# Optimization experiments

Measured on AMD Instinct MI355X. Metric: run time of the kernel, lower is better.

## Reference

```python
import jax, jax.numpy as jnp
import numpy as np
from jax import lax

D_MODEL = 1024
D_INNER = 2048   # expand * d_model
D_STATE = 16
D_CONV = 4
DT_RANK = 64     # ceil(d_model / 16)
B_SZ, L_SEQ = 2, 2048


def setup_inputs() -> dict:
    key = jax.random.key(0)
    ks = jax.random.split(key, 12)
    s = lambda *sh: 1.0 / np.sqrt(sh[-1])
    inp = {
        "x": jax.random.normal(ks[0], (B_SZ, L_SEQ, D_MODEL), jnp.float32),
        "in_proj_w": jax.random.normal(ks[1], (2 * D_INNER, D_MODEL), jnp.float32) * s(D_MODEL),
        "conv_w": jax.random.normal(ks[2], (D_INNER, 1, D_CONV), jnp.float32) * 0.3,
        "conv_b": jax.random.normal(ks[3], (D_INNER,), jnp.float32) * 0.05,
        "x_proj_w": jax.random.normal(ks[4], (DT_RANK + 2 * D_STATE, D_INNER), jnp.float32) * s(D_INNER),
        "dt_proj_w": jax.random.normal(ks[5], (D_INNER, DT_RANK), jnp.float32) * s(DT_RANK),
        "dt_proj_b": jnp.log(jnp.exp(jax.random.uniform(ks[6], (D_INNER,), jnp.float32, 1e-3, 1e-1)) - 1.0),
        "A_log": jnp.log(jnp.broadcast_to(jnp.arange(1, D_STATE + 1, dtype=jnp.float32), (D_INNER, D_STATE))),
        "D": jnp.ones((D_INNER,), jnp.float32),
        "out_proj_w": jax.random.normal(ks[7], (D_MODEL, D_INNER), jnp.float32) * s(D_INNER),
        "ln_w": jnp.ones((D_MODEL,), jnp.float32),
        "ln_b": jnp.zeros((D_MODEL,), jnp.float32),
    }
    return inp


def _mamba(x, in_proj_w, conv_w, conv_b, x_proj_w, dt_proj_w, dt_proj_b, A_log, D, out_proj_w):
    # x: [B, L, d_model]
    xz = x @ in_proj_w.T                             # [B, L, 2*d_inner]
    u, z = jnp.split(xz, 2, axis=-1)                 # [B, L, d_inner] each
    # depthwise causal conv1d along L
    u_c = jnp.swapaxes(u, 1, 2)                      # [B, d_inner, L]
    u_c = lax.conv_general_dilated(
        u_c, conv_w, window_strides=(1,), padding=[(D_CONV - 1, 0)],
        feature_group_count=D_INNER, dimension_numbers=("NCH", "OIH", "NCH"))
    u_c = u_c + conv_b[None, :, None]
    u_c = jax.nn.silu(jnp.swapaxes(u_c, 1, 2))       # [B, L, d_inner]
    # input-dependent dt, B, C
    x_dbl = u_c @ x_proj_w.T                         # [B, L, dt_rank + 2*d_state]
    dt_lr = x_dbl[..., :DT_RANK]
    Bm = x_dbl[..., DT_RANK:DT_RANK + D_STATE]       # [B, L, d_state]
    Cm = x_dbl[..., DT_RANK + D_STATE:]              # [B, L, d_state]
    dt = jax.nn.softplus(dt_lr @ dt_proj_w.T + dt_proj_b)  # [B, L, d_inner]
    A = -jnp.exp(A_log)                              # [d_inner, d_state]

    def step(h, inputs):
        dt_t, b_t, c_t, u_t = inputs                 # [B,d_inner],[B,N],[B,N],[B,d_inner]
        dA = jnp.exp(dt_t[:, :, None] * A)           # [B, d_inner, N]
        h = h * dA + (dt_t * u_t)[:, :, None] * b_t[:, None, :]
        y_t = jnp.einsum("bdn,bn->bd", h, c_t)
        return h, y_t

    h0 = jnp.zeros((x.shape[0], D_INNER, D_STATE), x.dtype)
    xs = (jnp.swapaxes(dt, 0, 1), jnp.swapaxes(Bm, 0, 1),
          jnp.swapaxes(Cm, 0, 1), jnp.swapaxes(u_c, 0, 1))
    _, ys = lax.scan(step, h0, xs)                   # ys: [L, B, d_inner]
    y = jnp.swapaxes(ys, 0, 1) + u_c * D             # skip connection D*u
    y = y * jax.nn.silu(z)                           # gate
    return y @ out_proj_w.T                          # [B, L, d_model]


def _layernorm(x, w, b, eps=1e-5):
    mu = jnp.mean(x, axis=-1, keepdims=True)
    var = jnp.mean(jnp.square(x - mu), axis=-1, keepdims=True)
    return (x - mu) * lax.rsqrt(var + eps) * w + b


def reference(x, in_proj_w, conv_w, conv_b, x_proj_w, dt_proj_w, dt_proj_b,
              A_log, D, out_proj_w, ln_w, ln_b):
    y = _mamba(x, in_proj_w, conv_w, conv_b, x_proj_w, dt_proj_w, dt_proj_b,
               A_log, D, out_proj_w)
    return _layernorm(y + x, ln_w, ln_b)  # dropout_level=0 -> identity
```

## Files before the change

### kernel.cpp

```cpp
#include <hip/hip_runtime.h>
#include <hip/hip_bf16.h>
#include <math.h>

#define DEV static __device__ __forceinline__

typedef __hip_bfloat16 bf16;
typedef __attribute__((ext_vector_type(8))) short bf16x8;
typedef __attribute__((ext_vector_type(4))) short bf16x4;
typedef __attribute__((ext_vector_type(4))) float f32x4;

static constexpr int D_MODEL = 1024;
static constexpr int D_INNER = 2048;
static constexpr int D_STATE = 16;
static constexpr int DT_RANK = 64;
static constexpr int B_SZ   = 2;
static constexpr int L_SEQ  = 2048;
static constexpr int T_TOK  = B_SZ * L_SEQ;
static constexpr int LC     = 64;
static constexpr int NC     = L_SEQ / LC;
static constexpr int NXP    = DT_RANK + 2 * D_STATE;
static constexpr int KSPLIT = 8;

static constexpr int P_CONVW = 0;
static constexpr int P_CONVB = 8192;
static constexpr int P_DTB   = 10240;
static constexpr int P_ALOG  = 12288;
static constexpr int P_DW    = 45056;
static constexpr int P_LNW   = 47104;
static constexpr int P_LNB   = 48128;
static constexpr int P_TOT   = 49152;

DEV float bf2f(bf16 x) { return __bfloat162float(x); }
DEV bf16  f2bf(float x) { return __float2bfloat16(x); }
DEV float sigmoidf_(float x) { return 1.0f / (1.0f + __expf(-x)); }
DEV float s2f(short s) { bf16 b; __builtin_memcpy(&b, &s, 2); return bf2f(b); }
DEV short f2s(float x) { bf16 b = f2bf(x); short s; __builtin_memcpy(&s, &b, 2); return s; }

DEV bool probe_f32(const unsigned short* probe) { return probe[1] == 0; }

DEV void async_copy16(const void* g, void* l) {
  __builtin_amdgcn_global_load_lds(
      (const __attribute__((address_space(1))) void*)g,
      (__attribute__((address_space(3))) void*)l, 16, 0, 0);
}

template <int N>
DEV void vm_wait() {
  if constexpr (N == 6) asm volatile("s_waitcnt vmcnt(6)" ::: "memory");
  else                  asm volatile("s_waitcnt vmcnt(0)" ::: "memory");
}

__global__ void cvt_all(const void* s0, const void* s1, const void* s2,
                        const void* s3, const void* s4,
                        const void* s5, const void* s6, const void* s7,
                        const void* s8, const void* s9, const void* s10,
                        const void* s11,
                        bf16* d0, bf16* d1, bf16* d2, bf16* d3, bf16* d4,
                        float* params,
                        const unsigned short* __restrict__ probe)
{
  long i = (long)(blockIdx.x * 256 + threadIdx.x) * 4;
  const void* src; long off;
  bf16* dstb = nullptr; float* dstf = nullptr;
  if      (i <  4194304) { src = s0;  dstb = d0; off = i; }
  else if (i <  8388608) { src = s1;  dstb = d1; off = i - 4194304; }
  else if (i <  8585216) { src = s2;  dstb = d2; off = i - 8388608; }
  else if (i <  8716288) { src = s3;  dstb = d3; off = i - 8585216; }
  else if (i < 10813440) { src = s4;  dstb = d4; off = i - 8716288; }
  else if (i < 10821632) { src = s5;  dstf = params + P_CONVW; off = i - 10813440; }
  else if (i < 10823680) { src = s6;  dstf = params + P_CONVB; off = i - 10821632; }
  else if (i < 10825728) { src = s7;  dstf = params + P_DTB;   off = i - 10823680; }
  else if (i < 10858496) { src = s8;  dstf = params + P_ALOG;  off = i - 10825728; }
  else if (i < 10860544) { src = s9;  dstf = params + P_DW;    off = i - 10858496; }
  else if (i < 10861568) { src = s10; dstf = params + P_LNW;   off = i - 10860544; }
  else if (i < 10862592) { src = s11; dstf = params + P_LNB;   off = i - 10861568; }
  else return;
  bool isf32 = probe_f32(probe);
  float v[4];
  if (isf32) {
    float4 t = *(const float4*)((const float*)src + off);
    v[0] = t.x; v[1] = t.y; v[2] = t.z; v[3] = t.w;
  } else {
    short4 t = *(const short4*)((const bf16*)src + off);
    v[0] = s2f(t.x); v[1] = s2f(t.y); v[2] = s2f(t.z); v[3] = s2f(t.w);
  }
  if (dstb) {
    #pragma unroll
    for (int k = 0; k < 4; ++k) dstb[off + k] = f2bf(v[k]);
  } else {
    #pragma unroll
    for (int k = 0; k < 4; ++k) dstf[off + k] = v[k];
  }
}

static constexpr int SLOT = 48 * 1024;
static constexpr int BOFF = 32 * 1024;

DEV void stage_A(const bf16* __restrict__ A, int ld, int bm, int k0,
                 char* slot, int tid) {
  #pragma unroll
  for (int j = 0; j < 4; ++j) {
    int p   = j * 8192 + tid * 16;
    int row = p >> 7;
    int ck  = ((p >> 4) & 7) ^ (row & 7);
    async_copy16(A + (size_t)(bm + row) * ld + k0 + ck * 8,
                 slot + j * 8192 + (tid >> 6) * 1024);
  }
}

DEV void stage_B(const bf16* __restrict__ B, int ld, int bn, int k0,
                 char* slot, int tid) {
  #pragma unroll
  for (int j = 0; j < 2; ++j) {
    int p   = j * 8192 + tid * 16;
    int row = p >> 7;
    int ck  = ((p >> 4) & 7) ^ (row & 7);
    async_copy16(B + (size_t)(bn + row) * ld + k0 + ck * 8,
                 slot + BOFF + j * 8192 + (tid >> 6) * 1024);
  }
}

template <int MODE>
DEV void gemm_pipe(const bf16* __restrict__ A, const bf16* __restrict__ B,
                   int M, int K, int ld,
                   void* __restrict__ o0, void* __restrict__ o1)
{
  __shared__ __align__(16) char ring[3 * SLOT];
  if (MODE == 3) {
    A += (size_t)blockIdx.z * K;
    B += (size_t)blockIdx.z * K;
  }
  const int tid  = threadIdx.x;
  const int wave = tid >> 6;
  const int lane = tid & 63;
  const int bm = blockIdx.x * 256;
  const int bn = blockIdx.y * 128;
  const int wm = (wave >> 1) * 64;
  const int wn = (wave & 1) * 64;
  const int fr = lane & 15;
  const int fq = lane >> 4;
  const int NT = K / 64;

  f32x4 acc[4][4];
  #pragma unroll
  for (int i = 0; i < 4; ++i)
    #pragma unroll
    for (int j = 0; j < 4; ++j)
      #pragma unroll
      for (int r = 0; r < 4; ++r) acc[i][j][r] = 0.0f;

  stage_A(A, ld, bm, 0,  ring,        tid);
  stage_B(B, ld, bn, 0,  ring,        tid);
  stage_A(A, ld, bm, 64, ring + SLOT, tid);
  stage_B(B, ld, bn, 64, ring + SLOT, tid);

  int scur = 0;
  #pragma unroll 1
  for (int tk = 0; tk < NT; ++tk) {
    if (tk < NT - 1) vm_wait<6>();
    else             vm_wait<0>();
    __builtin_amdgcn_sched_barrier(0);
    __builtin_amdgcn_s_barrier();
    __builtin_amdgcn_sched_barrier(0);

    const char* sa = ring + scur * SLOT;
    int snxt = scur + 2; if (snxt >= 3) snxt -= 3;
    char* sn = ring + snxt * SLOT;

    bf16x8 af[4][2], bg[2][2];
    #pragma unroll
    for (int mi = 0; mi < 4; ++mi)
      #pragma unroll
      for (int kk = 0; kk < 2; ++kk) {
        int row = wm + mi * 16 + fr;
        af[mi][kk] = *(const bf16x8*)(sa + row * 128 + (((kk * 4 + fq) ^ (fr & 7)) * 16));
      }
    #pragma unroll
    for (int ni = 0; ni < 2; ++ni)
      #pragma unroll
      for (int kk = 0; kk < 2; ++kk) {
        int row = wn + ni * 16 + fr;
        bg[ni][kk] = *(const bf16x8*)(sa + BOFF + row * 128 + (((kk * 4 + fq) ^ (fr & 7)) * 16));
      }
    __builtin_amdgcn_sched_barrier(0);
    if (tk + 2 < NT) stage_A(A, ld, bm, (tk + 2) * 64, sn, tid);
    __builtin_amdgcn_sched_barrier(0);
    asm volatile("s_waitcnt lgkmcnt(0)" ::: "memory");
    __builtin_amdgcn_sched_barrier(0);
    __builtin_amdgcn_s_setprio(1);
    #pragma unroll
    for (int kk = 0; kk < 2; ++kk)
      #pragma unroll
      for (int mi = 0; mi < 4; ++mi)
        #pragma unroll
        for (int ni = 0; ni < 2; ++ni)
          acc[mi][ni] = __builtin_amdgcn_mfma_f32_16x16x32_bf16(af[mi][kk], bg[ni][kk], acc[mi][ni], 0, 0, 0);
    __builtin_amdgcn_s_setprio(0);
    __builtin_amdgcn_sched_barrier(0);

    bf16x8 bh[2][2];
    #pragma unroll
    for (int ni = 0; ni < 2; ++ni)
      #pragma unroll
      for (int kk = 0; kk < 2; ++kk) {
        int row = wn + (ni + 2) * 16 + fr;
        bh[ni][kk] = *(const bf16x8*)(sa + BOFF + row * 128 + (((kk * 4 + fq) ^ (fr & 7)) * 16));
      }
    __builtin_amdgcn_sched_barrier(0);
    if (tk + 2 < NT) stage_B(B, ld, bn, (tk + 2) * 64, sn, tid);
    __builtin_amdgcn_sched_barrier(0);
    asm volatile("s_waitcnt lgkmcnt(0)" ::: "memory");
    __builtin_amdgcn_sched_barrier(0);
    __builtin_amdgcn_s_setprio(1);
    #pragma unroll
    for (int kk = 0; kk < 2; ++kk)
      #pragma unroll
      for (int mi = 0; mi < 4; ++mi)
        #pragma unroll
        for (int ni = 0; ni < 2; ++ni)
          acc[mi][ni + 2] = __builtin_amdgcn_mfma_f32_16x16x32_bf16(af[mi][kk], bh[ni][kk], acc[mi][ni + 2], 0, 0, 0);
    __builtin_amdgcn_s_setprio(0);
    __builtin_amdgcn_sched_barrier(0);

    scur = (scur + 1 == 3) ? 0 : scur + 1;
  }

  const int er = (lane >> 4) * 4;
  const int ec = lane & 15;
  #pragma unroll
  for (int mi = 0; mi < 4; ++mi) {
    #pragma unroll
    for (int ni = 0; ni < 4; ++ni) {
      #pragma unroll
      for (int r = 0; r < 4; ++r) {
        int row = bm + wm + mi * 16 + er + r;
        int col = bn + wn + ni * 16 + ec;
        float v = acc[mi][ni][r];
        if (MODE == 0) {
          if (col < D_INNER) ((bf16*)o0)[(size_t)row * D_INNER + col] = f2bf(v);
          else               ((bf16*)o1)[(size_t)row * D_INNER + (col - D_INNER)] = f2bf(v * sigmoidf_(v));
        } else {
          ((bf16*)o0)[((size_t)blockIdx.z * M + row) * D_MODEL + col] = f2bf(v);
        }
      }
    }
  }
}

template <int MODE>
DEV void gemm_body32(const bf16* __restrict__ A, const bf16* __restrict__ B,
                     int M, int N, int K, int ld,
                     void* __restrict__ o0, const void* __restrict__ e0)
{
  __shared__ __align__(16) bf16 As[128 * 32];
  __shared__ __align__(16) bf16 Bs[128 * 32];
  if (MODE == 1) {
    A += (size_t)blockIdx.z * K;
    B += (size_t)blockIdx.z * K;
  }
  const int tid  = threadIdx.x;
  const int wave = tid >> 6;
  const int lane = tid & 63;
  const int bm = blockIdx.x * 128;
  const int bn = blockIdx.y * 128;
  const int wm = (wave >> 1) * 64;
  const int wn = (wave & 1) * 64;

  f32x4 acc[4][4];
  #pragma unroll
  for (int i = 0; i < 4; ++i)
    #pragma unroll
    for (int j = 0; j < 4; ++j)
      #pragma unroll
      for (int r = 0; r < 4; ++r) acc[i][j][r] = 0.0f;

  const int ar0 = tid >> 2;
  const int ar1 = ar0 + 64;
  const int ac  = (tid & 3) * 8;
  const int fr = lane & 15;
  const int fk = (lane >> 4) * 8;

  for (int k0 = 0; k0 < K; k0 += 32) {
    bf16x8 a0 = *(const bf16x8*)(A + (size_t)(bm + ar0) * ld + k0 + ac);
    bf16x8 a1 = *(const bf16x8*)(A + (size_t)(bm + ar1) * ld + k0 + ac);
    int r0 = bn + ar0; if (r0 > N - 1) r0 = N - 1;
    int r1 = bn + ar1; if (r1 > N - 1) r1 = N - 1;
    bf16x8 b0 = *(const bf16x8*)(B + (size_t)r0 * ld + k0 + ac);
    bf16x8 b1 = *(const bf16x8*)(B + (size_t)r1 * ld + k0 + ac);
    __syncthreads();
    *(bf16x8*)(As + ar0 * 32 + ac) = a0;
    *(bf16x8*)(As + ar1 * 32 + ac) = a1;
    *(bf16x8*)(Bs + ar0 * 32 + ac) = b0;
    *(bf16x8*)(Bs + ar1 * 32 + ac) = b1;
    __syncthreads();

    bf16x8 af[4], bg[4];
    #pragma unroll
    for (int mi = 0; mi < 4; ++mi)
      af[mi] = *(const bf16x8*)(As + (wm + mi * 16 + fr) * 32 + fk);
    #pragma unroll
    for (int ni = 0; ni < 4; ++ni)
      bg[ni] = *(const bf16x8*)(Bs + (wn + ni * 16 + fr) * 32 + fk);
    #pragma unroll
    for (int mi = 0; mi < 4; ++mi)
      #pragma unroll
      for (int ni = 0; ni < 4; ++ni)
        acc[mi][ni] = __builtin_amdgcn_mfma_f32_16x16x32_bf16(af[mi], bg[ni], acc[mi][ni], 0, 0, 0);
  }

  const int er = (lane >> 4) * 4;
  const int ec = lane & 15;
  #pragma unroll
  for (int mi = 0; mi < 4; ++mi) {
    #pragma unroll
    for (int ni = 0; ni < 4; ++ni) {
      #pragma unroll
      for (int r = 0; r < 4; ++r) {
        int row = bm + wm + mi * 16 + er + r;
        int col = bn + wn + ni * 16 + ec;
        if (col >= N) continue;
        float v = acc[mi][ni][r];
        if (MODE == 1) {
          ((float*)o0)[((size_t)blockIdx.z * M + row) * N + col] = v;
        } else {
          v += ((const float*)e0)[col];
          float sp = (v > 15.0f) ? v : __logf(1.0f + __expf(v));
          ((bf16*)o0)[(size_t)row * D_INNER + col] = f2bf(sp);
        }
      }
    }
  }
}

__global__ void __launch_bounds__(512) k_inproj(const bf16* A, const bf16* B,
    void* o0, void* o1) {
  gemm_pipe<0>(A, B, T_TOK, D_MODEL, D_MODEL, o0, o1);
}
__global__ void __launch_bounds__(512) k_outproj(const bf16* A, const bf16* B,
    void* o0) {
  gemm_pipe<3>(A, B, T_TOK, D_INNER / 2, D_INNER, o0, nullptr);
}
__global__ void __launch_bounds__(256) k_xproj(const bf16* A, const bf16* B,
    void* o0) {
  gemm_body32<1>(A, B, T_TOK, NXP, D_INNER / KSPLIT, D_INNER, o0, nullptr);
}
__global__ void __launch_bounds__(256) k_dtproj(const bf16* A, const bf16* B,
    void* o0, const void* e0) {
  gemm_body32<2>(A, B, T_TOK, D_INNER, DT_RANK, DT_RANK, o0, e0);
}

__global__ void xproj_post(const float* __restrict__ partials,
                           bf16* __restrict__ dtlr,
                           float* __restrict__ Bbuf,
                           float* __restrict__ Cbuf)
{
  int i = blockIdx.x * 256 + threadIdx.x;
  int col = i % NXP;
  int row = i / NXP;
  float s = 0.0f;
  #pragma unroll
  for (int kz = 0; kz < KSPLIT; ++kz)
    s += partials[((size_t)kz * T_TOK + row) * NXP + col];
  if      (col < DT_RANK)            dtlr[(size_t)row * DT_RANK + col] = f2bf(s);
  else if (col < DT_RANK + D_STATE)  Bbuf[(size_t)row * D_STATE + (col - DT_RANK)] = s;
  else                               Cbuf[(size_t)row * D_STATE + (col - DT_RANK - D_STATE)] = s;
}

__global__ void conv_silu_kernel(const bf16* __restrict__ u_pre,
                                 const float* __restrict__ cw,
                                 const float* __restrict__ cb,
                                 bf16* __restrict__ uc_bf)
{
  int idx = blockIdx.x * 256 + threadIdx.x;
  int d4 = (idx * 4) & (D_INNER - 1);
  int t  = (idx * 4) >> 11;
  int l  = t & (L_SEQ - 1);
  float4 bias = *(const float4*)(cb + d4);
  float acc[4] = {bias.x, bias.y, bias.z, bias.w};
  float4 wv[4];
  #pragma unroll
  for (int i = 0; i < 4; ++i) wv[i] = *(const float4*)(cw + (d4 + i) * 4);
  #pragma unroll
  for (int w = 0; w < 4; ++w) {
    if (l - 3 + w >= 0) {
      bf16x4 u = *(const bf16x4*)(u_pre + (size_t)(t - 3 + w) * D_INNER + d4);
      float uf[4];
      #pragma unroll
      for (int i = 0; i < 4; ++i) { short su = u[i]; uf[i] = s2f(su); }
      acc[0] += uf[0] * ((const float*)&wv[0])[w];
      acc[1] += uf[1] * ((const float*)&wv[1])[w];
      acc[2] += uf[2] * ((const float*)&wv[2])[w];
      acc[3] += uf[3] * ((const float*)&wv[3])[w];
    }
  }
  bf16x4 out;
  #pragma unroll
  for (int i = 0; i < 4; ++i) out[i] = f2s(acc[i] * sigmoidf_(acc[i]));
  *(bf16x4*)(uc_bf + (size_t)t * D_INNER + d4) = out;
}

DEV void load_Ad(const float* A_log, int d, float* Ad, bool& fast) {
  fast = true;
  #pragma unroll
  for (int n = 0; n < 16; ++n) {
    Ad[n] = -__expf(A_log[d * 16 + n]);
    fast = fast && (fabsf(Ad[n] + (float)(n + 1)) < 1e-3f * (n + 1));
  }
}
DEV void compute_decay(bool fast, float dtv, const float* Ad, float* dec) {
  if (fast) {
    float e1 = __expf(-dtv);
    float en = e1;
    #pragma unroll
    for (int n = 0; n < 16; ++n) { dec[n] = en; en *= e1; }
  } else {
    #pragma unroll
    for (int n = 0; n < 16; ++n) dec[n] = __expf(Ad[n] * dtv);
  }
}

__global__ __launch_bounds__(256) void scan_pass1(
    const bf16* __restrict__ dt, const bf16* __restrict__ uc_bf,
    const float* __restrict__ Bbuf, const float* __restrict__ A_log,
    float* __restrict__ hend, float* __restrict__ sumdt)
{
  __shared__ float Bs4[LC * D_STATE];
  __shared__ bf16 dts[16 * 256];
  __shared__ bf16 uts[16 * 256];
  int bid = blockIdx.x;
  int tid = threadIdx.x;
  int dt8 = bid & 7;
  int c = (bid >> 3) & (NC - 1);
  int b = bid >> 8;
  int d0 = dt8 * 256;
  int d  = d0 + tid;
  int t0g = b * L_SEQ + c * LC;

  ((f32x4*)Bs4)[tid] = ((const f32x4*)(Bbuf + (size_t)t0g * D_STATE))[tid];

  float Ad[16], h[16];
  bool fast;
  load_Ad(A_log, d, Ad, fast);
  #pragma unroll
  for (int n = 0; n < 16; ++n) h[n] = 0.0f;
  float sdt = 0.0f;

  for (int sub = 0; sub < 4; ++sub) {
    __syncthreads();
    #pragma unroll
    for (int rep = 0; rep < 2; ++rep) {
      int idx = rep * 256 + tid;
      int row = idx >> 5;
      int col = (idx & 31) * 8;
      size_t src = (size_t)(t0g + sub * 16 + row) * D_INNER + d0 + col;
      *(bf16x8*)(dts + row * 256 + col) = *(const bf16x8*)(dt + src);
      *(bf16x8*)(uts + row * 256 + col) = *(const bf16x8*)(uc_bf + src);
    }
    __syncthreads();
    for (int t = 0; t < 16; ++t) {
      float dtv = bf2f(dts[t * 256 + tid]);
      float uv  = bf2f(uts[t * 256 + tid]);
      float su  = dtv * uv;
      sdt += dtv;
      float dec[16];
      compute_decay(fast, dtv, Ad, dec);
      const float* Bp = Bs4 + (sub * 16 + t) * 16;
      #pragma unroll
      for (int n = 0; n < 16; ++n)
        h[n] = h[n] * dec[n] + su * Bp[n];
    }
  }
  size_t base = ((size_t)(b * NC + c) * D_INNER + d) * 16;
  #pragma unroll
  for (int q = 0; q < 4; ++q)
    *(f32x4*)(hend + base + q * 4) = *(f32x4*)(h + q * 4);
  sumdt[(size_t)(b * NC + c) * D_INNER + d] = sdt;
}

__global__ __launch_bounds__(256) void scan_pass2(
    float* __restrict__ hend, const float* __restrict__ sumdt,
    const float* __restrict__ A_log)
{
  __shared__ float Ms[4][64];
  __shared__ float Es[4][64];
  int bid = blockIdx.x;
  int tid = threadIdx.x;
  int cg   = tid >> 6;
  int lane = tid & 63;
  int dloc = lane >> 4;
  int n    = lane & 15;
  int b     = bid >> 9;
  int d     = (bid & 511) * 4 + dloc;

  float a = -__expf(A_log[d * 16 + n]);

  float Ml[8], El[8];
  float M = 1.0f, E = 0.0f;
  #pragma unroll
  for (int j = 0; j < 8; ++j) {
    int c = cg * 8 + j;
    size_t sbase = (size_t)(b * NC + c) * D_INNER + d;
    float m = __expf(a * sumdt[sbase]);
    float e = hend[sbase * 16 + n];
    Ml[j] = M; El[j] = E;
    M = m * M;
    E = m * E + e;
  }
  Ms[cg][lane] = M;
  Es[cg][lane] = E;
  __syncthreads();
  float Ep = 0.0f;
  for (int g = 0; g < cg; ++g) {
    float Mg = Ms[g][lane], Eg = Es[g][lane];
    Ep = Mg * Ep + Eg;
  }
  #pragma unroll
  for (int j = 0; j < 8; ++j) {
    int c = cg * 8 + j;
    size_t sbase = (size_t)(b * NC + c) * D_INNER + d;
    hend[sbase * 16 + n] = Ml[j] * Ep + El[j];
  }
}

__global__ __launch_bounds__(256) void scan_pass3(
    const bf16* __restrict__ dt, const bf16* __restrict__ uc_bf,
    const float* __restrict__ Bbuf, const float* __restrict__ Cbuf,
    const bf16* __restrict__ z_silu, const float* __restrict__ hstart,
    const float* __restrict__ A_log, const float* __restrict__ Dw,
    bf16* __restrict__ y_bf)
{
  __shared__ float Bs4[LC * D_STATE];
  __shared__ float Cs4[LC * D_STATE];
  __shared__ bf16 dts[16 * 256];
  __shared__ bf16 uts[16 * 256];
  __shared__ bf16 zts[16 * 256];
  int bid = blockIdx.x;
  int tid = threadIdx.x;
  int dt8 = bid & 7;
  int c = (bid >> 3) & (NC - 1);
  int b = bid >> 8;
  int d0 = dt8 * 256;
  int d  = d0 + tid;
  int t0g = b * L_SEQ + c * LC;

  ((f32x4*)Bs4)[tid] = ((const f32x4*)(Bbuf + (size_t)t0g * D_STATE))[tid];
  ((f32x4*)Cs4)[tid] = ((const f32x4*)(Cbuf + (size_t)t0g * D_STATE))[tid];

  float Ad[16], h[16];
  bool fast;
  load_Ad(A_log, d, Ad, fast);
  size_t base = ((size_t)(b * NC + c) * D_INNER + d) * 16;
  #pragma unroll
  for (int q = 0; q < 4; ++q)
    *(f32x4*)(h + q * 4) = *(const f32x4*)(hstart + base + q * 4);
  float Dv = Dw[d];

  for (int sub = 0; sub < 4; ++sub) {
    __syncthreads();
    #pragma unroll
    for (int rep = 0; rep < 2; ++rep) {
      int idx = rep * 256 + tid;
      int row = idx >> 5;
      int col = (idx & 31) * 8;
      size_t src = (size_t)(t0g + sub * 16 + row) * D_INNER + d0 + col;
      *(bf16x8*)(dts + row * 256 + col) = *(const bf16x8*)(dt + src);
      *(bf16x8*)(uts + row * 256 + col) = *(const bf16x8*)(uc_bf + src);
      *(bf16x8*)(zts + row * 256 + col) = *(const bf16x8*)(z_silu + src);
    }
    __syncthreads();
    for (int t = 0; t < 16; ++t) {
      float dtv = bf2f(dts[t * 256 + tid]);
      float uv  = bf2f(uts[t * 256 + tid]);
      float zv  = bf2f(zts[t * 256 + tid]);
      float su  = dtv * uv;
      float dec[16];
      compute_decay(fast, dtv, Ad, dec);
      const float* Bp = Bs4 + (sub * 16 + t) * 16;
      const float* Cp = Cs4 + (sub * 16 + t) * 16;
      float y = 0.0f;
      #pragma unroll
      for (int n = 0; n < 16; ++n) {
        h[n] = h[n] * dec[n] + su * Bp[n];
        y += h[n] * Cp[n];
      }
      y = (y + uv * Dv) * zv;
      y_bf[(size_t)(t0g + sub * 16 + t) * D_INNER + d] = f2bf(y);
    }
  }
}

__global__ void ln_kernel(const bf16* __restrict__ parts,
                          const bf16* __restrict__ x_bf,
                          const float* __restrict__ w,
                          const float* __restrict__ bia,
                          void* __restrict__ out,
                          const unsigned short* __restrict__ probe)
{
  int t = blockIdx.x;
  int tid = threadIdx.x;
  const bf16* p0 = parts + (size_t)t * D_MODEL;
  const bf16* p1 = parts + ((size_t)T_TOK + t) * D_MODEL;
  const bf16* xr = x_bf + (size_t)t * D_MODEL;
  float v[4];
  float s = 0.0f, q = 0.0f;
  #pragma unroll
  for (int k = 0; k < 4; ++k) {
    int col = tid + k * 256;
    v[k] = bf2f(p0[col]) + bf2f(p1[col]) + bf2f(xr[col]);
    s += v[k]; q += v[k] * v[k];
  }
  #pragma unroll
  for (int off = 32; off >= 1; off >>= 1) {
    s += __shfl_down(s, off);
    q += __shfl_down(q, off);
  }
  __shared__ float red[8];
  __shared__ float mv[2];
  int wave = tid >> 6, lane = tid & 63;
  if (lane == 0) { red[wave] = s; red[4 + wave] = q; }
  __syncthreads();
  if (tid == 0) {
    float S = red[0] + red[1] + red[2] + red[3];
    float Q = red[4] + red[5] + red[6] + red[7];
    float mu = S * (1.0f / D_MODEL);
    float var = Q * (1.0f / D_MODEL) - mu * mu;
    mv[0] = mu; mv[1] = rsqrtf(var + 1e-5f);
  }
  __syncthreads();
  float mu = mv[0], rs = mv[1];
  bool isf32 = probe_f32(probe);
  #pragma unroll
  for (int k = 0; k < 4; ++k) {
    int col = tid + k * 256;
    float r = (v[k] - mu) * rs * w[col] + bia[col];
    if (isf32) ((float*)out)[(size_t)t * D_MODEL + col] = r;
    else       ((bf16*) out)[(size_t)t * D_MODEL + col] = f2bf(r);
  }
}

extern "C" void kernel_launch(void* const* d_in, const int* in_sizes, int n_in,
                              void* d_out, int out_size, void* d_ws, size_t ws_size,
                              hipStream_t stream)
{
  const void* x        = d_in[0];
  const void* in_w     = d_in[1];
  const void* conv_w   = d_in[2];
  const void* conv_b   = d_in[3];
  const void* xproj_w  = d_in[4];
  const void* dtproj_w = d_in[5];
  const void* dtproj_b = d_in[6];
  const void* A_log    = d_in[7];
  const void* Dw       = d_in[8];
  const void* out_w    = d_in[9];
  const void* ln_w     = d_in[10];
  const void* ln_b     = d_in[11];
  const unsigned short* probe = (const unsigned short*)A_log;

  char* p = (char*)d_ws;
  auto alloc = [&](size_t bytes) { char* r = p; p += (bytes + 255) & ~255ull; return r; };
  bf16*  x_bf   = (bf16*) alloc((size_t)T_TOK * D_MODEL * 2);
  bf16*  inw_bf = (bf16*) alloc((size_t)2 * D_INNER * D_MODEL * 2);
  bf16*  xpw_bf = (bf16*) alloc((size_t)NXP * D_INNER * 2);
  bf16*  dtw_bf = (bf16*) alloc((size_t)D_INNER * DT_RANK * 2);
  bf16*  outw_bf= (bf16*) alloc((size_t)D_MODEL * D_INNER * 2);
  float* params = (float*)alloc((size_t)P_TOT * 4);
  bf16*  u_pre  = (bf16*) alloc((size_t)T_TOK * D_INNER * 2);
  bf16*  z_silu = (bf16*) alloc((size_t)T_TOK * D_INNER * 2);
  bf16*  uc_bf  = (bf16*) alloc((size_t)T_TOK * D_INNER * 2);
  bf16*  dtlr   = (bf16*) alloc((size_t)T_TOK * DT_RANK * 2);
  float* Bbuf   = (float*)alloc((size_t)T_TOK * D_STATE * 4);
  float* Cbuf   = (float*)alloc((size_t)T_TOK * D_STATE * 4);
  bf16*  dtb    = (bf16*) alloc((size_t)T_TOK * D_INNER * 2);
  float* hend   = (float*)alloc((size_t)B_SZ * NC * D_INNER * 16 * 4);
  float* sumdt  = (float*)alloc((size_t)B_SZ * NC * D_INNER * 4);
  bf16*  y_bf   = u_pre;
  float* xparts = (float*)dtb;
  bf16*  oparts = z_silu;

  dim3 blk(256);
  dim3 blk512(512);
  cvt_all<<<10608, blk, 0, stream>>>(x, in_w, xproj_w, dtproj_w, out_w,
                                     conv_w, conv_b, dtproj_b, A_log, Dw, ln_w, ln_b,
                                     x_bf, inw_bf, xpw_bf, dtw_bf, outw_bf, params, probe);

  k_inproj<<<dim3(T_TOK / 256, (2 * D_INNER) / 128), blk512, 0, stream>>>(x_bf, inw_bf, u_pre, z_silu);
  conv_silu_kernel<<<(T_TOK * D_INNER) / 1024, blk, 0, stream>>>(u_pre, params + P_CONVW, params + P_CONVB, uc_bf);
  k_xproj<<<dim3(T_TOK / 128, 1, KSPLIT), blk, 0, stream>>>(uc_bf, xpw_bf, xparts);
  xproj_post<<<(T_TOK * NXP) / 256, blk, 0, stream>>>(xparts, dtlr, Bbuf, Cbuf);
  k_dtproj<<<dim3(T_TOK / 128, D_INNER / 128), blk, 0, stream>>>(dtlr, dtw_bf, dtb, params + P_DTB);
  scan_pass1<<<B_SZ * NC * (D_INNER / 256), blk, 0, stream>>>(dtb, uc_bf, Bbuf, params + P_ALOG, hend, sumdt);
  scan_pass2<<<(B_SZ * D_INNER) / 2, blk, 0, stream>>>(hend, sumdt, params + P_ALOG);
  scan_pass3<<<B_SZ * NC * (D_INNER / 256), blk, 0, stream>>>(
      dtb, uc_bf, Bbuf, Cbuf, z_silu, hend, params + P_ALOG, params + P_DW, y_bf);
  k_outproj<<<dim3(T_TOK / 256, D_MODEL / 128, 2), blk512, 0, stream>>>(y_bf, outw_bf, oparts);
  ln_kernel<<<T_TOK, blk, 0, stream>>>(oparts, x_bf, params + P_LNW, params + P_LNB, d_out, probe);
}
```

Before: 307.7 us.

## Fuse causal conv+SiLU into in_proj epilogue and xproj reduction into dt_proj

The in_proj GEMM epilogue for the u half now stages its tile in shared memory and applies the depthwise causal conv, bias and SiLU directly. The three halo rows at the tile boundary are recomputed with a scalar dot product over K. Separately, the x_proj split-K reduction is merged into a new dt_proj MFMA kernel that also writes B and C, and the weight conversion kernel is widened to 8 elements per thread. This removes the u_pre and dtlr round-trips and two launches, at the cost of a serial 1024-long halo dot product in some in_proj blocks.

```diff
diff --git a/kernel.cpp b/kernel.cpp
--- a/kernel.cpp
+++ b/kernel.cpp
@@ -59,7 +59,7 @@
                         float* params,
                         const unsigned short* __restrict__ probe)
 {
-  long i = (long)(blockIdx.x * 256 + threadIdx.x) * 4;
+  long i = (long)(blockIdx.x * 256 + threadIdx.x) * 8;
   const void* src; long off;
   bf16* dstb = nullptr; float* dstf = nullptr;
   if      (i <  4194304) { src = s0;  dstb = d0; off = i; }
@@ -76,20 +76,27 @@
   else if (i < 10862592) { src = s11; dstf = params + P_LNB;   off = i - 10861568; }
   else return;
   bool isf32 = probe_f32(probe);
-  float v[4];
+  float v[8];
   if (isf32) {
-    float4 t = *(const float4*)((const float*)src + off);
-    v[0] = t.x; v[1] = t.y; v[2] = t.z; v[3] = t.w;
+    float4 a = *(const float4*)((const float*)src + off);
+    float4 b = *(const float4*)((const float*)src + off + 4);
+    v[0]=a.x; v[1]=a.y; v[2]=a.z; v[3]=a.w;
+    v[4]=b.x; v[5]=b.y; v[6]=b.z; v[7]=b.w;
   } else {
-    short4 t = *(const short4*)((const bf16*)src + off);
-    v[0] = s2f(t.x); v[1] = s2f(t.y); v[2] = s2f(t.z); v[3] = s2f(t.w);
+    bf16x8 t = *(const bf16x8*)((const bf16*)src + off);
+    #pragma unroll
+    for (int k = 0; k < 8; ++k) { short sk = t[k]; v[k] = s2f(sk); }
   }
   if (dstb) {
-    #pragma unroll
-    for (int k = 0; k < 4; ++k) dstb[off + k] = f2bf(v[k]);
+    bf16x8 o;
+    #pragma unroll
+    for (int k = 0; k < 8; ++k) o[k] = f2s(v[k]);
+    *(bf16x8*)(dstb + off) = o;
   } else {
-    #pragma unroll
-    for (int k = 0; k < 4; ++k) dstf[off + k] = v[k];
+    f32x4 a = {v[0], v[1], v[2], v[3]};
+    f32x4 b = {v[4], v[5], v[6], v[7]};
+    *(f32x4*)(dstf + off)     = a;
+    *(f32x4*)(dstf + off + 4) = b;
   }
 }
 
@@ -123,9 +130,12 @@
 template <int MODE>
 DEV void gemm_pipe(const bf16* __restrict__ A, const bf16* __restrict__ B,
                    int M, int K, int ld,
-                   void* __restrict__ o0, void* __restrict__ o1)
+                   void* __restrict__ o0, void* __restrict__ o1,
+                   const float* __restrict__ cw, const float* __restrict__ cb)
 {
   __shared__ __align__(16) char ring[3 * SLOT];
+  const bf16* Aorig = A;
+  const bf16* Borig = B;
   if (MODE == 3) {
     A += (size_t)blockIdx.z * K;
     B += (size_t)blockIdx.z * K;
@@ -227,42 +237,114 @@
 
   const int er = (lane >> 4) * 4;
   const int ec = lane & 15;
-  #pragma unroll
-  for (int mi = 0; mi < 4; ++mi) {
-    #pragma unroll
-    for (int ni = 0; ni < 4; ++ni) {
-      #pragma unroll
-      for (int r = 0; r < 4; ++r) {
-        int row = bm + wm + mi * 16 + er + r;
-        int col = bn + wn + ni * 16 + ec;
-        float v = acc[mi][ni][r];
-        if (MODE == 0) {
-          if (col < D_INNER) ((bf16*)o0)[(size_t)row * D_INNER + col] = f2bf(v);
-          else               ((bf16*)o1)[(size_t)row * D_INNER + (col - D_INNER)] = f2bf(v * sigmoidf_(v));
-        } else {
-          ((bf16*)o0)[((size_t)blockIdx.z * M + row) * D_MODEL + col] = f2bf(v);
+
+  if (MODE == 3) {
+    #pragma unroll
+    for (int mi = 0; mi < 4; ++mi)
+      #pragma unroll
+      for (int ni = 0; ni < 4; ++ni)
+        #pragma unroll
+        for (int r = 0; r < 4; ++r) {
+          int row = bm + wm + mi * 16 + er + r;
+          int col = bn + wn + ni * 16 + ec;
+          ((bf16*)o0)[((size_t)blockIdx.z * M + row) * D_MODEL + col] = f2bf(acc[mi][ni][r]);
         }
+    return;
+  }
+
+  if (bn >= D_INNER) {
+    #pragma unroll
+    for (int mi = 0; mi < 4; ++mi)
+      #pragma unroll
+      for (int ni = 0; ni < 4; ++ni)
+        #pragma unroll
+        for (int r = 0; r < 4; ++r) {
+          int row = bm + wm + mi * 16 + er + r;
+          int col = bn + wn + ni * 16 + ec - D_INNER;
+          float v = acc[mi][ni][r];
+          ((bf16*)o1)[(size_t)row * D_INNER + col] = f2bf(v * sigmoidf_(v));
+        }
+    return;
+  }
+
+  __syncthreads();
+  bf16*  uT  = (bf16*)ring;
+  float* cws = (float*)(ring + 70656);
+  float* cbs = (float*)(ring + 72704);
+
+  #pragma unroll
+  for (int mi = 0; mi < 4; ++mi)
+    #pragma unroll
+    for (int ni = 0; ni < 4; ++ni)
+      #pragma unroll
+      for (int r = 0; r < 4; ++r)
+        uT[(size_t)(wm + mi * 16 + er + r + 3) * 136 + wn + ni * 16 + ec] = f2bf(acc[mi][ni][r]);
+
+  if (tid < 128) {
+    *(f32x4*)(cws + tid * 4) = *(const f32x4*)(cw + (size_t)(bn + tid) * 4);
+    cbs[tid] = cb[bn + tid];
+  }
+
+  if ((bm & (L_SEQ - 1)) != 0 && tid < 384) {
+    int j = tid >> 7;
+    int c = tid & 127;
+    const bf16* xr = Aorig + (size_t)(bm - 3 + j) * ld;
+    const bf16* wr = Borig + (size_t)(bn + c) * ld;
+    float s = 0.0f;
+    for (int k8 = 0; k8 < 1024; k8 += 8) {
+      bf16x8 xa = *(const bf16x8*)(xr + k8);
+      bf16x8 wb = *(const bf16x8*)(wr + k8);
+      #pragma unroll
+      for (int q = 0; q < 8; ++q) { short a = xa[q], b = wb[q]; s += s2f(a) * s2f(b); }
+    }
+    uT[(size_t)j * 136 + c] = f2bf(s);
+  }
+  __syncthreads();
+
+  const int cg = tid & 15;
+  float cwr[4][8], cbr[8];
+  #pragma unroll
+  for (int i = 0; i < 8; ++i) {
+    f32x4 w4 = *(const f32x4*)(cws + (cg * 8 + i) * 4);
+    cwr[0][i] = w4[0]; cwr[1][i] = w4[1]; cwr[2][i] = w4[2]; cwr[3][i] = w4[3];
+    cbr[i] = cbs[cg * 8 + i];
+  }
+  const int lbase = bm & (L_SEQ - 1);
+  #pragma unroll
+  for (int j = 0; j < 8; ++j) {
+    int row = (tid >> 4) + j * 32;
+    float a8[8];
+    #pragma unroll
+    for (int i = 0; i < 8; ++i) a8[i] = cbr[i];
+    #pragma unroll
+    for (int w = 0; w < 4; ++w) {
+      if (lbase + row - 3 + w >= 0) {
+        bf16x8 u8 = *(const bf16x8*)(uT + (size_t)(row + w) * 136 + cg * 8);
+        #pragma unroll
+        for (int i = 0; i < 8; ++i) { short uu = u8[i]; a8[i] += s2f(uu) * cwr[w][i]; }
       }
     }
-  }
-}
-
-template <int MODE>
-DEV void gemm_body32(const bf16* __restrict__ A, const bf16* __restrict__ B,
-                     int M, int N, int K, int ld,
-                     void* __restrict__ o0, const void* __restrict__ e0)
+    bf16x8 o;
+    #pragma unroll
+    for (int i = 0; i < 8; ++i) o[i] = f2s(a8[i] * sigmoidf_(a8[i]));
+    *(bf16x8*)((bf16*)o0 + (size_t)(bm + row) * D_INNER + bn + cg * 8) = o;
+  }
+}
+
+__global__ void __launch_bounds__(256) k_xproj(const bf16* __restrict__ A,
+                                               const bf16* __restrict__ B,
+                                               float* __restrict__ o0)
 {
   __shared__ __align__(16) bf16 As[128 * 32];
   __shared__ __align__(16) bf16 Bs[128 * 32];
-  if (MODE == 1) {
-    A += (size_t)blockIdx.z * K;
-    B += (size_t)blockIdx.z * K;
-  }
+  const int M = T_TOK, N = NXP, K = D_INNER / KSPLIT, ld = D_INNER;
+  A += (size_t)blockIdx.z * K;
+  B += (size_t)blockIdx.z * K;
   const int tid  = threadIdx.x;
   const int wave = tid >> 6;
   const int lane = tid & 63;
   const int bm = blockIdx.x * 128;
-  const int bn = blockIdx.y * 128;
+  const int bn = 0;
   const int wm = (wave >> 1) * 64;
   const int wn = (wave & 1) * 64;
 
@@ -311,92 +393,126 @@
   const int er = (lane >> 4) * 4;
   const int ec = lane & 15;
   #pragma unroll
-  for (int mi = 0; mi < 4; ++mi) {
-    #pragma unroll
-    for (int ni = 0; ni < 4; ++ni) {
+  for (int mi = 0; mi < 4; ++mi)
+    #pragma unroll
+    for (int ni = 0; ni < 4; ++ni)
       #pragma unroll
       for (int r = 0; r < 4; ++r) {
         int row = bm + wm + mi * 16 + er + r;
         int col = bn + wn + ni * 16 + ec;
         if (col >= N) continue;
-        float v = acc[mi][ni][r];
-        if (MODE == 1) {
-          ((float*)o0)[((size_t)blockIdx.z * M + row) * N + col] = v;
-        } else {
-          v += ((const float*)e0)[col];
-          float sp = (v > 15.0f) ? v : __logf(1.0f + __expf(v));
-          ((bf16*)o0)[(size_t)row * D_INNER + col] = f2bf(sp);
-        }
+        o0[((size_t)blockIdx.z * M + row) * N + col] = acc[mi][ni][r];
       }
-    }
-  }
 }
 
 __global__ void __launch_bounds__(512) k_inproj(const bf16* A, const bf16* B,
-    void* o0, void* o1) {
-  gemm_pipe<0>(A, B, T_TOK, D_MODEL, D_MODEL, o0, o1);
+    void* o0, void* o1, const float* cw, const float* cb) {
+  gemm_pipe<0>(A, B, T_TOK, D_MODEL, D_MODEL, o0, o1, cw, cb);
 }
 __global__ void __launch_bounds__(512) k_outproj(const bf16* A, const bf16* B,
     void* o0) {
-  gemm_pipe<3>(A, B, T_TOK, D_INNER / 2, D_INNER, o0, nullptr);
-}
-__global__ void __launch_bounds__(256) k_xproj(const bf16* A, const bf16* B,
-    void* o0) {
-  gemm_body32<1>(A, B, T_TOK, NXP, D_INNER / KSPLIT, D_INNER, o0, nullptr);
-}
-__global__ void __launch_bounds__(256) k_dtproj(const bf16* A, const bf16* B,
-    void* o0, const void* e0) {
-  gemm_body32<2>(A, B, T_TOK, D_INNER, DT_RANK, DT_RANK, o0, e0);
-}
-
-__global__ void xproj_post(const float* __restrict__ partials,
-                           bf16* __restrict__ dtlr,
-                           float* __restrict__ Bbuf,
-                           float* __restrict__ Cbuf)
+  gemm_pipe<3>(A, B, T_TOK, D_INNER / 2, D_INNER, o0, nullptr, nullptr, nullptr);
+}
+
+__global__ __launch_bounds__(256) void k_dtfuse(
+    const float* __restrict__ partials,
+    const bf16*  __restrict__ dtw,
+    const float* __restrict__ dtbias,
+    float* __restrict__ Bbuf, float* __restrict__ Cbuf,
+    bf16* __restrict__ dtb)
 {
-  int i = blockIdx.x * 256 + threadIdx.x;
-  int col = i % NXP;
-  int row = i / NXP;
-  float s = 0.0f;
-  #pragma unroll
-  for (int kz = 0; kz < KSPLIT; ++kz)
-    s += partials[((size_t)kz * T_TOK + row) * NXP + col];
-  if      (col < DT_RANK)            dtlr[(size_t)row * DT_RANK + col] = f2bf(s);
-  else if (col < DT_RANK + D_STATE)  Bbuf[(size_t)row * D_STATE + (col - DT_RANK)] = s;
-  else                               Cbuf[(size_t)row * D_STATE + (col - DT_RANK - D_STATE)] = s;
-}
-
-__global__ void conv_silu_kernel(const bf16* __restrict__ u_pre,
-                                 const float* __restrict__ cw,
-                                 const float* __restrict__ cb,
-                                 bf16* __restrict__ uc_bf)
-{
-  int idx = blockIdx.x * 256 + threadIdx.x;
-  int d4 = (idx * 4) & (D_INNER - 1);
-  int t  = (idx * 4) >> 11;
-  int l  = t & (L_SEQ - 1);
-  float4 bias = *(const float4*)(cb + d4);
-  float acc[4] = {bias.x, bias.y, bias.z, bias.w};
-  float4 wv[4];
-  #pragma unroll
-  for (int i = 0; i < 4; ++i) wv[i] = *(const float4*)(cw + (d4 + i) * 4);
-  #pragma unroll
-  for (int w = 0; w < 4; ++w) {
-    if (l - 3 + w >= 0) {
-      bf16x4 u = *(const bf16x4*)(u_pre + (size_t)(t - 3 + w) * D_INNER + d4);
-      float uf[4];
-      #pragma unroll
-      for (int i = 0; i < 4; ++i) { short su = u[i]; uf[i] = s2f(su); }
-      acc[0] += uf[0] * ((const float*)&wv[0])[w];
-      acc[1] += uf[1] * ((const float*)&wv[1])[w];
-      acc[2] += uf[2] * ((const float*)&wv[2])[w];
-      acc[3] += uf[3] * ((const float*)&wv[3])[w];
+  __shared__ __align__(16) bf16 Al[128 * 72];
+  __shared__ __align__(16) bf16 Bl[128 * 72];
+  const int tid = threadIdx.x;
+  unsigned lin = blockIdx.x + gridDim.x * blockIdx.y;
+  unsigned nid = (lin & 7) * 64 + (lin >> 3);
+  const int cblk = nid & 15;
+  const int tblk = nid >> 4;
+  const int r0 = tblk * 128;
+  const int c0 = cblk * 128;
+
+  #pragma unroll
+  for (int it = 0; it < 8; ++it) {
+    int idx = it * 256 + tid;
+    int row = idx >> 4;
+    int g   = idx & 15;
+    f32x4 s = {0.0f, 0.0f, 0.0f, 0.0f};
+    #pragma unroll
+    for (int kz = 0; kz < KSPLIT; ++kz)
+      s += *(const f32x4*)(partials + ((size_t)kz * T_TOK + r0 + row) * NXP + g * 4);
+    bf16x4 o;
+    #pragma unroll
+    for (int k = 0; k < 4; ++k) o[k] = f2s(s[k]);
+    *(bf16x4*)(Al + row * 72 + g * 4) = o;
+  }
+  if (cblk == 0) {
+    #pragma unroll
+    for (int it = 0; it < 4; ++it) {
+      int idx = it * 256 + tid;
+      int row = idx >> 3;
+      int g   = 16 + (idx & 7);
+      f32x4 s = {0.0f, 0.0f, 0.0f, 0.0f};
+      #pragma unroll
+      for (int kz = 0; kz < KSPLIT; ++kz)
+        s += *(const f32x4*)(partials + ((size_t)kz * T_TOK + r0 + row) * NXP + g * 4);
+      if (g < 20) *(f32x4*)(Bbuf + (size_t)(r0 + row) * D_STATE + (g - 16) * 4) = s;
+      else        *(f32x4*)(Cbuf + (size_t)(r0 + row) * D_STATE + (g - 20) * 4) = s;
     }
   }
-  bf16x4 out;
-  #pragma unroll
-  for (int i = 0; i < 4; ++i) out[i] = f2s(acc[i] * sigmoidf_(acc[i]));
-  *(bf16x4*)(uc_bf + (size_t)t * D_INNER + d4) = out;
+  #pragma unroll
+  for (int it = 0; it < 4; ++it) {
+    int idx = it * 256 + tid;
+    int row = idx >> 3;
+    int cv  = (idx & 7) * 8;
+    *(bf16x8*)(Bl + row * 72 + cv) = *(const bf16x8*)(dtw + (size_t)(c0 + row) * 64 + cv);
+  }
+  __syncthreads();
+
+  const int wave = tid >> 6;
+  const int lane = tid & 63;
+  const int wm = (wave >> 1) * 64;
+  const int wn = (wave & 1) * 64;
+  const int fr = lane & 15;
+  const int fk = (lane >> 4) * 8;
+  const int er = (lane >> 4) * 4;
+  const int ec = lane & 15;
+
+  f32x4 acc[4][4];
+  #pragma unroll
+  for (int i = 0; i < 4; ++i)
+    #pragma unroll
+    for (int j = 0; j < 4; ++j)
+      #pragma unroll
+      for (int r = 0; r < 4; ++r) acc[i][j][r] = 0.0f;
+
+  #pragma unroll
+  for (int k0 = 0; k0 < 64; k0 += 32) {
+    bf16x8 af[4], bg[4];
+    #pragma unroll
+    for (int mi = 0; mi < 4; ++mi)
+      af[mi] = *(const bf16x8*)(Al + (wm + mi * 16 + fr) * 72 + k0 + fk);
+    #pragma unroll
+    for (int ni = 0; ni < 4; ++ni)
+      bg[ni] = *(const bf16x8*)(Bl + (wn + ni * 16 + fr) * 72 + k0 + fk);
+    #pragma unroll
+    for (int mi = 0; mi < 4; ++mi)
+      #pragma unroll
+      for (int ni = 0; ni < 4; ++ni)
+        acc[mi][ni] = __builtin_amdgcn_mfma_f32_16x16x32_bf16(af[mi], bg[ni], acc[mi][ni], 0, 0, 0);
+  }
+
+  #pragma unroll
+  for (int mi = 0; mi < 4; ++mi)
+    #pragma unroll
+    for (int ni = 0; ni < 4; ++ni)
+      #pragma unroll
+      for (int r = 0; r < 4; ++r) {
+        int orow = r0 + wm + mi * 16 + er + r;
+        int ocol = c0 + wn + ni * 16 + ec;
+        float v = acc[mi][ni][r] + dtbias[ocol];
+        float sp = (v > 15.0f) ? v : __logf(1.0f + __expf(v));
+        dtb[(size_t)orow * D_INNER + ocol] = f2bf(sp);
+      }
 }
 
 DEV void load_Ad(const float* A_log, int d, float* Ad, bool& fast) {
@@ -664,30 +780,28 @@
   bf16*  dtw_bf = (bf16*) alloc((size_t)D_INNER * DT_RANK * 2);
   bf16*  outw_bf= (bf16*) alloc((size_t)D_MODEL * D_INNER * 2);
   float* params = (float*)alloc((size_t)P_TOT * 4);
-  bf16*  u_pre  = (bf16*) alloc((size_t)T_TOK * D_INNER * 2);
+  bf16*  scratch= (bf16*) alloc((size_t)T_TOK * D_INNER * 2);
   bf16*  z_silu = (bf16*) alloc((size_t)T_TOK * D_INNER * 2);
   bf16*  uc_bf  = (bf16*) alloc((size_t)T_TOK * D_INNER * 2);
-  bf16*  dtlr   = (bf16*) alloc((size_t)T_TOK * DT_RANK * 2);
   float* Bbuf   = (float*)alloc((size_t)T_TOK * D_STATE * 4);
   float* Cbuf   = (float*)alloc((size_t)T_TOK * D_STATE * 4);
   bf16*  dtb    = (bf16*) alloc((size_t)T_TOK * D_INNER * 2);
   float* hend   = (float*)alloc((size_t)B_SZ * NC * D_INNER * 16 * 4);
   float* sumdt  = (float*)alloc((size_t)B_SZ * NC * D_INNER * 4);
-  bf16*  y_bf   = u_pre;
-  float* xparts = (float*)dtb;
+  float* xparts = (float*)scratch;
+  bf16*  y_bf   = scratch;
   bf16*  oparts = z_silu;
 
   dim3 blk(256);
   dim3 blk512(512);
-  cvt_all<<<10608, blk, 0, stream>>>(x, in_w, xproj_w, dtproj_w, out_w,
-                                     conv_w, conv_b, dtproj_b, A_log, Dw, ln_w, ln_b,
-                                     x_bf, inw_bf, xpw_bf, dtw_bf, outw_bf, params, probe);
-
-  k_inproj<<<dim3(T_TOK / 256, (2 * D_INNER) / 128), blk512, 0, stream>>>(x_bf, inw_bf, u_pre, z_silu);
-  conv_silu_kernel<<<(T_TOK * D_INNER) / 1024, blk, 0, stream>>>(u_pre, params + P_CONVW, params + P_CONVB, uc_bf);
+  cvt_all<<<5304, blk, 0, stream>>>(x, in_w, xproj_w, dtproj_w, out_w,
+                                    conv_w, conv_b, dtproj_b, A_log, Dw, ln_w, ln_b,
+                                    x_bf, inw_bf, xpw_bf, dtw_bf, outw_bf, params, probe);
+
+  k_inproj<<<dim3(T_TOK / 256, (2 * D_INNER) / 128), blk512, 0, stream>>>(
+      x_bf, inw_bf, uc_bf, z_silu, params + P_CONVW, params + P_CONVB);
   k_xproj<<<dim3(T_TOK / 128, 1, KSPLIT), blk, 0, stream>>>(uc_bf, xpw_bf, xparts);
-  xproj_post<<<(T_TOK * NXP) / 256, blk, 0, stream>>>(xparts, dtlr, Bbuf, Cbuf);
-  k_dtproj<<<dim3(T_TOK / 128, D_INNER / 128), blk, 0, stream>>>(dtlr, dtw_bf, dtb, params + P_DTB);
+  k_dtfuse<<<dim3(16, 32), blk, 0, stream>>>(xparts, dtw_bf, params + P_DTB, Bbuf, Cbuf, dtb);
   scan_pass1<<<B_SZ * NC * (D_INNER / 256), blk, 0, stream>>>(dtb, uc_bf, Bbuf, params + P_ALOG, hend, sumdt);
   scan_pass2<<<(B_SZ * D_INNER) / 2, blk, 0, stream>>>(hend, sumdt, params + P_ALOG);
   scan_pass3<<<B_SZ * NC * (D_INNER / 256), blk, 0, stream>>>(
```

After: 294.6 us. -4.2%, faster.
